# Optimization experiments

Hardware: AMD Instinct MI355X
Metric: run time of the kernel (lower is better)

Reference implementation:

```python
import jax, jax.numpy as jnp
import numpy as np

B, D, H, W, C = 2, 8, 64, 64, 128
NH = 8
WS = (2, 8, 8)
SS = (1, 4, 4)
HEAD_DIM = C // NH
SCALE = HEAD_DIM ** -0.5
MLP_HIDDEN = 4 * C


def _window_partition(x, ws):
    # x: (B, D, H, W, C) -> (B*nW, ws0*ws1*ws2, C)
    b, d, h, w, c = x.shape
    x = x.reshape(b, d // ws[0], ws[0], h // ws[1], ws[1], w // ws[2], ws[2], c)
    return x.transpose(0, 1, 3, 5, 2, 4, 6, 7).reshape(-1, ws[0] * ws[1] * ws[2], c)


def _window_reverse(win, ws, b, d, h, w):
    x = win.reshape(b, d // ws[0], h // ws[1], w // ws[2], ws[0], ws[1], ws[2], -1)
    return x.transpose(0, 1, 4, 2, 5, 3, 6, 7).reshape(b, d, h, w, -1)


def _rel_pos_index(ws):
    coords = np.stack(np.meshgrid(np.arange(ws[0]), np.arange(ws[1]), np.arange(ws[2]), indexing='ij'))
    cf = coords.reshape(3, -1)                       # (3, N)
    rel = (cf[:, :, None] - cf[:, None, :]).transpose(1, 2, 0)  # (N, N, 3)
    rel[:, :, 0] += ws[0] - 1
    rel[:, :, 1] += ws[1] - 1
    rel[:, :, 2] += ws[2] - 1
    rel[:, :, 0] *= (2 * ws[1] - 1) * (2 * ws[2] - 1)
    rel[:, :, 1] *= 2 * ws[2] - 1
    return rel.sum(-1)                               # (N, N)


def _attn_mask(d, h, w, ws, ss):
    img = np.zeros((1, d, h, w, 1), np.float32)
    cnt = 0
    for sd in (slice(-ws[0]), slice(-ws[0], -ss[0]), slice(-ss[0], None)):
        for sh in (slice(-ws[1]), slice(-ws[1], -ss[1]), slice(-ss[1], None)):
            for sw in (slice(-ws[2]), slice(-ws[2], -ss[2]), slice(-ss[2], None)):
                img[:, sd, sh, sw, :] = cnt
                cnt += 1
    mw = _window_partition(img, ws)[..., 0]          # (nW, N)
    am = mw[:, None, :] - mw[:, :, None]             # (nW, N, N)
    return np.where(am != 0, -100.0, 0.0).astype(np.float32)


def _ln(x, g, b):
    m = x.mean(-1, keepdims=True)
    v = ((x - m) ** 2).mean(-1, keepdims=True)
    return (x - m) / jnp.sqrt(v + 1e-5) * g + b


def setup_inputs() -> dict:
    key = jax.random.key(0)
    ks = jax.random.split(key, 8)
    n_bias = (2 * WS[0] - 1) * (2 * WS[1] - 1) * (2 * WS[2] - 1)
    return {
        'x': jax.random.normal(ks[0], (B, D, H, W, C), jnp.float32),
        'qkv_w': jax.random.normal(ks[1], (3 * C, C), jnp.float32) * 0.02,
        'qkv_b': jnp.zeros((3 * C,), jnp.float32),
        'proj_w': jax.random.normal(ks[2], (C, C), jnp.float32) * 0.02,
        'proj_b': jnp.zeros((C,), jnp.float32),
        'rpb': jax.random.normal(ks[3], (n_bias, NH), jnp.float32) * 0.02,
        'ln1_g': jnp.ones((C,), jnp.float32),
        'ln1_b': jnp.zeros((C,), jnp.float32),
        'ln2_g': jnp.ones((C,), jnp.float32),
        'ln2_b': jnp.zeros((C,), jnp.float32),
        'fc1_w': jax.random.normal(ks[4], (MLP_HIDDEN, C), jnp.float32) * 0.02,
        'fc1_b': jnp.zeros((MLP_HIDDEN,), jnp.float32),
        'fc2_w': jax.random.normal(ks[5], (C, MLP_HIDDEN), jnp.float32) * 0.02,
        'fc2_b': jnp.zeros((C,), jnp.float32),
    }


def reference(x, qkv_w, qkv_b, proj_w, proj_b, rpb, ln1_g, ln1_b, ln2_g, ln2_b, fc1_w, fc1_b, fc2_w, fc2_b):
    shortcut = x
    xn = _ln(x, ln1_g, ln1_b)
    # cyclic shift (SW-MSA)
    xs = jnp.roll(xn, (-SS[0], -SS[1], -SS[2]), axis=(1, 2, 3))
    win = _window_partition(xs, WS)                  # (Bw, N, C)
    Bw, N, _ = win.shape
    qkv = (win @ qkv_w.T + qkv_b).reshape(Bw, N, 3, NH, HEAD_DIM).transpose(2, 0, 3, 1, 4)
    q, k, v = qkv[0] * SCALE, qkv[1], qkv[2]         # (Bw, NH, N, d)
    attn = jnp.einsum('bhnd,bhmd->bhnm', q, k)       # (Bw, NH, N, N)
    rpi = _rel_pos_index(WS)
    bias = rpb[rpi.reshape(-1)].reshape(N, N, NH).transpose(2, 0, 1)  # (NH, N, N)
    attn = attn + bias[None]
    mask = jnp.asarray(_attn_mask(D, H, W, WS, SS))  # (nW, N, N)
    nW = mask.shape[0]
    attn = attn.reshape(B, nW, NH, N, N) + mask[None, :, None]
    attn = jax.nn.softmax(attn, axis=-1).reshape(Bw, NH, N, N)
    out = jnp.einsum('bhnm,bhmd->bhnd', attn, v).transpose(0, 2, 1, 3).reshape(Bw, N, C)
    out = out @ proj_w.T + proj_b
    xr = _window_reverse(out, WS, B, D, H, W)
    xr = jnp.roll(xr, SS, axis=(1, 2, 3))
    x1 = shortcut + xr
    # MLP block
    y = _ln(x1, ln2_g, ln2_b)
    y = jax.nn.gelu(y @ fc1_w.T + fc1_b, approximate=False)
    y = y @ fc2_w.T + fc2_b
    return x1 + y
```

## Files before the change

### kernel.cpp

```cpp
#include <hip/hip_runtime.h>
#include <math.h>

typedef short s16x8 __attribute__((ext_vector_type(8)));
typedef float f32x4 __attribute__((ext_vector_type(4)));

#define MFMA(a, b, c)   __builtin_amdgcn_mfma_f32_16x16x32_bf16(a, b, c, 0, 0, 0)

__device__ __forceinline__ float b2f(ushort u) {
    union { unsigned int i; float f; } v; v.i = ((unsigned int)u) << 16; return v.f;
}
__device__ __forceinline__ ushort f2b(float f) {
    union { float f; unsigned int i; } v; v.f = f;
    unsigned int r = v.i + 0x7fffu + ((v.i >> 16) & 1u);
    return (ushort)(r >> 16);
}
__device__ __forceinline__ float gelu_tanh(float v) {
    float u = 0.7978845608f * (v + 0.044715f * v * v * v);
    float e = __expf(-2.f * fabsf(u));
    float t = (1.f - e) / (1.f + e);
    t = (u < 0.f) ? -t : t;
    return 0.5f * v * (1.f + t);
}

__global__ __launch_bounds__(256) void k0_prep(
    const float* __restrict__ qkv_w, const float* __restrict__ proj_w,
    const float* __restrict__ fc1_w, const float* __restrict__ fc2_w,
    const float* __restrict__ rpb, ushort* __restrict__ wq,
    ushort* __restrict__ wp, ushort* __restrict__ wf, ushort* __restrict__ bm)
{
    int bid = blockIdx.x, tid = threadIdx.x;
    if (bid < 192) { int idx = bid * 256 + tid; wq[idx] = f2b(qkv_w[idx]); return; }
    if (bid < 256) { int idx = (bid - 192) * 256 + tid; wp[idx] = f2b(proj_w[idx]); return; }
    if (bid < 768) {
        int idx = (bid - 256) * 256 + tid;
        wf[idx] = f2b(idx < 65536 ? fc1_w[idx] : fc2_w[idx - 65536]);
        return;
    }
    int bi = bid - 768;
    int cls = bi >> 3, head = bi & 7;
    int ed = (cls >> 2) & 1, eh = (cls >> 1) & 1, ew = cls & 1;
    int j = tid & 127;
    int tdj = j >> 6, thj = (j >> 3) & 7, twj = j & 7;
    int regj = (ed ? (tdj + 1) : 0) * 9
             + (eh ? ((thj < 4) ? 1 : 2) : 0) * 3
             + (ew ? ((twj < 4) ? 1 : 2) : 0);
    ushort* bmp = bm + (long)bi * 16384;
    for (int ii = 0; ii < 64; ++ii) {
        int i = (tid >> 7) * 64 + ii;
        int tdi = i >> 6, thi = (i >> 3) & 7, twi = i & 7;
        int regi = (ed ? (tdi + 1) : 0) * 9
                 + (eh ? ((thi < 4) ? 1 : 2) : 0) * 3
                 + (ew ? ((twi < 4) ? 1 : 2) : 0);
        int rpi = (tdi - tdj + 1) * 225 + (thi - thj + 7) * 15 + (twi - twj + 7);
        float v = rpb[rpi * 8 + head] + ((regi != regj) ? -100.f : 0.f);
        bmp[i * 128 + j] = f2b(v);
    }
}

__global__ __launch_bounds__(256) void k2_qkv(
    const float* __restrict__ x, const float* __restrict__ g,
    const float* __restrict__ be, const ushort* __restrict__ wq,
    const float* __restrict__ qkv_b, ushort* __restrict__ qkv)
{
    __shared__ __align__(16) ushort As[128][136];
    int tid = threadIdx.x;
    int m0 = blockIdx.x * 128;
    {
        int row = tid >> 1, half = tid & 1;
        int tk = m0 + row;
        int wi = tk >> 7, t = tk & 127;
        int b = wi >> 8, wd = (wi >> 6) & 3, wh = (wi >> 3) & 7, ww = wi & 7;
        int td = t >> 6, th = (t >> 3) & 7, tw = t & 7;
        int d = (wd * 2 + td + 1) & 7;
        int h = (wh * 8 + th + 4) & 63;
        int w = (ww * 8 + tw + 4) & 63;
        long src = (((long)((b * 8 + d) * 64 + h)) * 64 + w) * 128 + half * 64;
        float vals[64];
        float s = 0.f, q = 0.f;
        #pragma unroll
        for (int i = 0; i < 16; ++i) {
            float4 u = *(const float4*)&x[src + i * 4];
            vals[i * 4 + 0] = u.x; vals[i * 4 + 1] = u.y;
            vals[i * 4 + 2] = u.z; vals[i * 4 + 3] = u.w;
            s += u.x + u.y + u.z + u.w;
            q += u.x * u.x + u.y * u.y + u.z * u.z + u.w * u.w;
        }
        s += __shfl_xor(s, 1);
        q += __shfl_xor(q, 1);
        float mean = s * (1.f / 128.f);
        float rstd = rsqrtf(q * (1.f / 128.f) - mean * mean + 1e-5f);
        #pragma unroll
        for (int i = 0; i < 8; ++i) {
            ushort pk[8];
            #pragma unroll
            for (int jj = 0; jj < 8; ++jj) {
                int c = half * 64 + i * 8 + jj;
                pk[jj] = f2b((vals[i * 8 + jj] - mean) * rstd * g[c] + be[c]);
            }
            *(uint4*)&As[row][half * 64 + i * 8] = *(uint4*)pk;
        }
    }
    __syncthreads();
    int wv = tid >> 6, lane = tid & 63, li = lane & 15, quad = lane >> 4;
    int wm = wv >> 1, wn = wv & 1;
    long wibase = (long)(m0 >> 7) * 49152;
    for (int nb = 0; nb < 3; ++nb) {
        f32x4 acc[4][4] = {};
        for (int s = 0; s < 4; ++s) {
            s16x8 a[4], bw[4];
            #pragma unroll
            for (int mi = 0; mi < 4; ++mi)
                a[mi] = *(const s16x8*)&As[wm * 64 + mi * 16 + li][s * 32 + quad * 8];
            #pragma unroll
            for (int ni = 0; ni < 4; ++ni)
                bw[ni] = *(const s16x8*)&wq[(long)(nb * 128 + wn * 64 + ni * 16 + li) * 128
                                            + s * 32 + quad * 8];
            #pragma unroll
            for (int mi = 0; mi < 4; ++mi)
                #pragma unroll
                for (int ni = 0; ni < 4; ++ni)
                    acc[mi][ni] = MFMA(a[mi], bw[ni], acc[mi][ni]);
        }
        #pragma unroll
        for (int mi = 0; mi < 4; ++mi)
            #pragma unroll
            for (int ni = 0; ni < 4; ++ni) {
                int gcol = nb * 128 + wn * 64 + ni * 16 + li;
                int mat = gcol >> 7, hd = (gcol >> 4) & 7;
                float bias = qkv_b[gcol];
                float scale = (mat == 0) ? 0.25f : 1.f;
                long base2 = wibase + mat * 16384 + hd * 2048 + li;
                #pragma unroll
                for (int r = 0; r < 4; ++r) {
                    int trow = wm * 64 + mi * 16 + quad * 4 + r;
                    qkv[base2 + trow * 16] = f2b((acc[mi][ni][r] + bias) * scale);
                }
            }
    }
}

__global__ __launch_bounds__(256) void k3_attn(
    ushort* __restrict__ qkv, const ushort* __restrict__ bm)
{
    __shared__ __align__(16) ushort qs[128][40];
    __shared__ __align__(16) ushort ks[128][40];
    __shared__ __align__(16) ushort vt[16][136];
    __shared__ __align__(16) ushort ps[128][136];
    int wi = blockIdx.x;
    int wd = (wi >> 6) & 3, wh = (wi >> 3) & 7, ww = wi & 7;
    int cls = ((wd == 3) << 2) | ((wh == 7) << 1) | (ww == 7);
    int tid = threadIdx.x;
    int wv = tid >> 6, lane = tid & 63, li = lane & 15, quad = lane >> 4;
    long wbase = (long)wi * 49152;
    uint2 opk[8][2];
    for (int h = 0; h < 8; ++h) {
        __syncthreads();
        {   int token = tid >> 1, dd0 = (tid & 1) * 8;
            long tb = wbase + h * 2048 + token * 16 + dd0;
            uint4 qv = *(const uint4*)&qkv[tb];
            uint4 kv = *(const uint4*)&qkv[tb + 16384];
            uint4 vv = *(const uint4*)&qkv[tb + 32768];
            uint4 z = {0, 0, 0, 0};
            *(uint4*)&qs[token][dd0] = qv;
            *(uint4*)&ks[token][dd0] = kv;
            *(uint4*)&qs[token][16 + dd0] = z;
            *(uint4*)&ks[token][16 + dd0] = z;
            const ushort* pv = (const ushort*)&vv;
            #pragma unroll
            for (int j = 0; j < 8; ++j) vt[dd0 + j][token] = pv[j];
        }
        __syncthreads();
        f32x4 sacc[2][8] = {};
        s16x8 a[2];
        #pragma unroll
        for (int mi = 0; mi < 2; ++mi)
            a[mi] = *(const s16x8*)&qs[wv * 32 + mi * 16 + li][quad * 8];
        #pragma unroll
        for (int ni = 0; ni < 8; ++ni) {
            s16x8 bf = *(const s16x8*)&ks[ni * 16 + li][quad * 8];
            #pragma unroll
            for (int mi = 0; mi < 2; ++mi) sacc[mi][ni] = MFMA(a[mi], bf, sacc[mi][ni]);
        }
        long bmbase = (long)(cls * 8 + h) * 16384;
        #pragma unroll
        for (int mi = 0; mi < 2; ++mi) {
            #pragma unroll
            for (int r = 0; r < 4; ++r) {
                int i = wv * 32 + mi * 16 + quad * 4 + r;
                float sv[8];
                float rowmax = -1e30f;
                #pragma unroll
                for (int ni = 0; ni < 8; ++ni) {
                    float v = sacc[mi][ni][r] + b2f(bm[bmbase + i * 128 + ni * 16 + li]);
                    sv[ni] = v;
                    rowmax = fmaxf(rowmax, v);
                }
                #pragma unroll
                for (int m = 1; m < 16; m <<= 1) rowmax = fmaxf(rowmax, __shfl_xor(rowmax, m));
                float sum = 0.f;
                #pragma unroll
                for (int ni = 0; ni < 8; ++ni) { sv[ni] = __expf(sv[ni] - rowmax); sum += sv[ni]; }
                #pragma unroll
                for (int m = 1; m < 16; m <<= 1) sum += __shfl_xor(sum, m);
                float inv = 1.f / sum;
                #pragma unroll
                for (int ni = 0; ni < 8; ++ni) ps[i][ni * 16 + li] = f2b(sv[ni] * inv);
            }
        }
        __syncthreads();
        f32x4 pacc[2] = {};
        #pragma unroll
        for (int kk = 0; kk < 4; ++kk) {
            s16x8 bv = *(const s16x8*)&vt[li][kk * 32 + quad * 8];
            #pragma unroll
            for (int mi = 0; mi < 2; ++mi) {
                s16x8 ap = *(const s16x8*)&ps[wv * 32 + mi * 16 + li][kk * 32 + quad * 8];
                pacc[mi] = MFMA(ap, bv, pacc[mi]);
            }
        }
        #pragma unroll
        for (int mi = 0; mi < 2; ++mi) {
            opk[h][mi].x = (unsigned int)f2b(pacc[mi][0]) | ((unsigned int)f2b(pacc[mi][1]) << 16);
            opk[h][mi].y = (unsigned int)f2b(pacc[mi][2]) | ((unsigned int)f2b(pacc[mi][3]) << 16);
        }
    }
    #pragma unroll
    for (int h = 0; h < 8; ++h)
        #pragma unroll
        for (int mi = 0; mi < 2; ++mi) {
            unsigned int w0 = opk[h][mi].x, w1 = opk[h][mi].y;
            #pragma unroll
            for (int r = 0; r < 4; ++r) {
                unsigned int word = (r < 2) ? w0 : w1;
                ushort v = (ushort)((word >> ((r & 1) * 16)) & 0xffff);
                int i = wv * 32 + mi * 16 + quad * 4 + r;
                qkv[wbase + (long)i * 128 + h * 16 + li] = v;
            }
        }
}

__global__ __launch_bounds__(256) void k45(
    const ushort* __restrict__ ao, const ushort* __restrict__ wp,
    const float* __restrict__ proj_b, const float* __restrict__ x,
    const float* __restrict__ g2, const float* __restrict__ be2,
    const ushort* __restrict__ wf1, const float* __restrict__ fc1_b,
    const ushort* __restrict__ wf2, const float* __restrict__ fc2_b,
    float* __restrict__ out)
{
    __shared__ __align__(16) ushort As[64][132];
    __shared__ __align__(16) ushort x1t[64][132];
    __shared__ __align__(16) ushort hs[64][132];
    __shared__ float redS[4][64];
    __shared__ float redQ[4][64];
    int tid = threadIdx.x;
    int b = blockIdx.x;
    int wi = b >> 1, half64 = b & 1;
    int wd = (wi >> 6) & 3, wh = (wi >> 3) & 7, ww = wi & 7;
    int bb = wi >> 8;
    long aobase = (long)wi * 49152 + half64 * 8192;
    #pragma unroll
    for (int i = 0; i < 4; ++i) {
        int slot = tid + i * 256;
        int row = slot >> 4, c8 = (slot & 15) * 8;
        *(uint4*)&As[row][c8] = *(const uint4*)&ao[aobase + row * 128 + c8];
    }
    __syncthreads();
    int wv = tid >> 6, lane = tid & 63, li = lane & 15, quad = lane >> 4;
    int wm = wv >> 1, wn = wv & 1;
    f32x4 acc[2][4] = {};
    for (int s = 0; s < 4; ++s) {
        s16x8 a[2], bw[4];
        #pragma unroll
        for (int mi = 0; mi < 2; ++mi)
            a[mi] = *(const s16x8*)&As[wm * 32 + mi * 16 + li][s * 32 + quad * 8];
        #pragma unroll
        for (int ni = 0; ni < 4; ++ni)
            bw[ni] = *(const s16x8*)&wp[(long)(wn * 64 + ni * 16 + li) * 128 + s * 32 + quad * 8];
        #pragma unroll
        for (int mi = 0; mi < 2; ++mi)
            #pragma unroll
            for (int ni = 0; ni < 4; ++ni)
                acc[mi][ni] = MFMA(a[mi], bw[ni], acc[mi][ni]);
    }
    #pragma unroll
    for (int mi = 0; mi < 2; ++mi) {
        #pragma unroll
        for (int r = 0; r < 4; ++r) {
            int lrow = wm * 32 + mi * 16 + quad * 4 + r;
            int t = half64 * 64 + lrow;
            int td = t >> 6, th = (t >> 3) & 7, tw = t & 7;
            int d = (wd * 2 + td + 1) & 7, h = (wh * 8 + th + 4) & 63, w = (ww * 8 + tw + 4) & 63;
            long di = (((long)((bb * 8 + d) * 64 + h)) * 64 + w) * 128;
            #pragma unroll
            for (int ni = 0; ni < 4; ++ni) {
                int col = wn * 64 + ni * 16 + li;
                x1t[lrow][col] = f2b(acc[mi][ni][r] + proj_b[col] + x[di + col]);
            }
        }
    }
    __syncthreads();
    {
        int token = tid & 63, part = tid >> 6;
        float vals[32];
        float s = 0.f, q = 0.f;
        #pragma unroll
        for (int i = 0; i < 4; ++i) {
            uint4 u = *(const uint4*)&x1t[token][part * 32 + i * 8];
            const ushort* p = (const ushort*)&u;
            #pragma unroll
            for (int j = 0; j < 8; ++j) { float f = b2f(p[j]); vals[i * 8 + j] = f; s += f; q += f * f; }
        }
        redS[part][token] = s; redQ[part][token] = q;
        __syncthreads();
        float st = 0.f, qt = 0.f;
        #pragma unroll
        for (int p2 = 0; p2 < 4; ++p2) { st += redS[p2][token]; qt += redQ[p2][token]; }
        float mean = st * (1.f / 128.f);
        float rstd = rsqrtf(qt * (1.f / 128.f) - mean * mean + 1e-5f);
        #pragma unroll
        for (int i = 0; i < 4; ++i) {
            ushort packed[8];
            #pragma unroll
            for (int j = 0; j < 8; ++j) {
                int c = part * 32 + i * 8 + j;
                packed[j] = f2b((vals[i * 8 + j] - mean) * rstd * g2[c] + be2[c]);
            }
            *(uint4*)&As[token][part * 32 + i * 8] = *(uint4*)packed;
        }
    }
    __syncthreads();
    f32x4 yacc[2][4] = {};
    for (int hc = 0; hc < 4; ++hc) {
        f32x4 hacc[2][4] = {};
        #pragma unroll
        for (int kk = 0; kk < 4; ++kk) {
            s16x8 a[2], bw[4];
            #pragma unroll
            for (int mi = 0; mi < 2; ++mi)
                a[mi] = *(const s16x8*)&As[wm * 32 + mi * 16 + li][kk * 32 + quad * 8];
            #pragma unroll
            for (int ni = 0; ni < 4; ++ni)
                bw[ni] = *(const s16x8*)&wf1[(long)(hc * 128 + wn * 64 + ni * 16 + li) * 128
                                             + kk * 32 + quad * 8];
            #pragma unroll
            for (int mi = 0; mi < 2; ++mi)
                #pragma unroll
                for (int ni = 0; ni < 4; ++ni)
                    hacc[mi][ni] = MFMA(a[mi], bw[ni], hacc[mi][ni]);
        }
        #pragma unroll
        for (int mi = 0; mi < 2; ++mi)
            #pragma unroll
            for (int ni = 0; ni < 4; ++ni) {
                int col = wn * 64 + ni * 16 + li;
                float bbv = fc1_b[hc * 128 + col];
                #pragma unroll
                for (int r = 0; r < 4; ++r) {
                    int row = wm * 32 + mi * 16 + quad * 4 + r;
                    hs[row][col] = f2b(gelu_tanh(hacc[mi][ni][r] + bbv));
                }
            }
        __syncthreads();
        #pragma unroll
        for (int kk = 0; kk < 4; ++kk) {
            s16x8 a[2], bw[4];
            #pragma unroll
            for (int mi = 0; mi < 2; ++mi)
                a[mi] = *(const s16x8*)&hs[wm * 32 + mi * 16 + li][kk * 32 + quad * 8];
            #pragma unroll
            for (int ni = 0; ni < 4; ++ni)
                bw[ni] = *(const s16x8*)&wf2[(long)(wn * 64 + ni * 16 + li) * 512
                                             + hc * 128 + kk * 32 + quad * 8];
            #pragma unroll
            for (int mi = 0; mi < 2; ++mi)
                #pragma unroll
                for (int ni = 0; ni < 4; ++ni)
                    yacc[mi][ni] = MFMA(a[mi], bw[ni], yacc[mi][ni]);
        }
        __syncthreads();
    }
    #pragma unroll
    for (int mi = 0; mi < 2; ++mi) {
        #pragma unroll
        for (int r = 0; r < 4; ++r) {
            int lrow = wm * 32 + mi * 16 + quad * 4 + r;
            int t = half64 * 64 + lrow;
            int td = t >> 6, th = (t >> 3) & 7, tw = t & 7;
            int d = (wd * 2 + td + 1) & 7, h = (wh * 8 + th + 4) & 63, w = (ww * 8 + tw + 4) & 63;
            long di = (((long)((bb * 8 + d) * 64 + h)) * 64 + w) * 128;
            #pragma unroll
            for (int ni = 0; ni < 4; ++ni) {
                int col = wn * 64 + ni * 16 + li;
                out[di + col] = b2f(x1t[lrow][col]) + yacc[mi][ni][r] + fc2_b[col];
            }
        }
    }
}

extern "C" void kernel_launch(void* const* d_in, const int* in_sizes, int n_in,
                              void* d_out, int out_size, void* d_ws, size_t ws_size,
                              hipStream_t stream)
{
    (void)in_sizes; (void)n_in; (void)out_size; (void)ws_size;
    const float* x      = (const float*)d_in[0];
    const float* qkv_w  = (const float*)d_in[1];
    const float* qkv_b  = (const float*)d_in[2];
    const float* proj_w = (const float*)d_in[3];
    const float* proj_b = (const float*)d_in[4];
    const float* rpb    = (const float*)d_in[5];
    const float* ln1_g  = (const float*)d_in[6];
    const float* ln1_b  = (const float*)d_in[7];
    const float* ln2_g  = (const float*)d_in[8];
    const float* ln2_b  = (const float*)d_in[9];
    const float* fc1_w  = (const float*)d_in[10];
    const float* fc1_b  = (const float*)d_in[11];
    const float* fc2_w  = (const float*)d_in[12];
    const float* fc2_b  = (const float*)d_in[13];
    float* out = (float*)d_out;

    ushort* qkvb = (ushort*)d_ws;
    ushort* wq   = (ushort*)((char*)d_ws + 50331648);
    ushort* wp   = wq + 49152;
    ushort* wf   = wp + 16384;
    ushort* bm   = wf + 131072;

    hipLaunchKernelGGL(k0_prep, dim3(832), dim3(256), 0, stream,
                       qkv_w, proj_w, fc1_w, fc2_w, rpb, wq, wp, wf, bm);
    hipLaunchKernelGGL(k2_qkv, dim3(512), dim3(256), 0, stream,
                       x, ln1_g, ln1_b, wq, qkv_b, qkvb);
    hipLaunchKernelGGL(k3_attn, dim3(512), dim3(256), 0, stream, qkvb, bm);
    hipLaunchKernelGGL(k45, dim3(1024), dim3(256), 0, stream,
                       qkvb, wp, proj_b, x, ln2_g, ln2_b,
                       wf, fc1_b, wf + 65536, fc2_b, out);
}
```

Baseline: 286.5 us.

## Compute LN2 stats from MFMA registers and keep x1 in registers

The proj+MLP kernel now computes the residual x1 in MFMA accumulator registers and reduces LayerNorm sums with wavefront shuffles plus a small shared buffer, instead of staging x1 through a shared tile and re-reading it. x1 is kept packed as bf16 in registers for the final residual add. The x1t shared array is removed and launch bounds request 4 blocks per CU. This cuts shared memory use and one sync, aiming at higher occupancy, but register pressure rises and spills become possible under the 4-block bound.

```diff
diff --git a/kernel.cpp b/kernel.cpp
--- a/kernel.cpp
+++ b/kernel.cpp
@@ -239,7 +239,7 @@
         }
 }
 
-__global__ __launch_bounds__(256) void k45(
+__global__ __launch_bounds__(256, 4) void k45(
     const ushort* __restrict__ ao, const ushort* __restrict__ wp,
     const float* __restrict__ proj_b, const float* __restrict__ x,
     const float* __restrict__ g2, const float* __restrict__ be2,
@@ -248,10 +248,9 @@
     float* __restrict__ out)
 {
     __shared__ __align__(16) ushort As[64][132];
-    __shared__ __align__(16) ushort x1t[64][132];
     __shared__ __align__(16) ushort hs[64][132];
-    __shared__ float redS[4][64];
-    __shared__ float redQ[4][64];
+    __shared__ float redS[2][64];
+    __shared__ float redQ[2][64];
     int tid = threadIdx.x;
     int b = blockIdx.x;
     int wi = b >> 1, half64 = b & 1;
@@ -282,52 +281,67 @@
             for (int ni = 0; ni < 4; ++ni)
                 acc[mi][ni] = MFMA(a[mi], bw[ni], acc[mi][ni]);
     }
+    int cols[4];
     #pragma unroll
-    for (int mi = 0; mi < 2; ++mi) {
-        #pragma unroll
-        for (int r = 0; r < 4; ++r) {
-            int lrow = wm * 32 + mi * 16 + quad * 4 + r;
-            int t = half64 * 64 + lrow;
-            int td = t >> 6, th = (t >> 3) & 7, tw = t & 7;
-            int d = (wd * 2 + td + 1) & 7, h = (wh * 8 + th + 4) & 63, w = (ww * 8 + tw + 4) & 63;
-            long di = (((long)((bb * 8 + d) * 64 + h)) * 64 + w) * 128;
-            #pragma unroll
-            for (int ni = 0; ni < 4; ++ni) {
-                int col = wn * 64 + ni * 16 + li;
-                x1t[lrow][col] = f2b(acc[mi][ni][r] + proj_b[col] + x[di + col]);
+    for (int ni = 0; ni < 4; ++ni) cols[ni] = wn * 64 + ni * 16 + li;
+    {
+        float pbv[4];
+        #pragma unroll
+        for (int ni = 0; ni < 4; ++ni) pbv[ni] = proj_b[cols[ni]];
+        #pragma unroll
+        for (int mi = 0; mi < 2; ++mi) {
+            #pragma unroll
+            for (int r = 0; r < 4; ++r) {
+                int lrow = wm * 32 + mi * 16 + quad * 4 + r;
+                int t = half64 * 64 + lrow;
+                int td = t >> 6, th = (t >> 3) & 7, tw = t & 7;
+                int d = (wd * 2 + td + 1) & 7, h = (wh * 8 + th + 4) & 63, w = (ww * 8 + tw + 4) & 63;
+                long di = (((long)((bb * 8 + d) * 64 + h)) * 64 + w) * 128;
+                float s_ = 0.f, q_ = 0.f;
+                #pragma unroll
+                for (int ni = 0; ni < 4; ++ni) {
+                    float v = acc[mi][ni][r] + pbv[ni] + x[di + cols[ni]];
+                    acc[mi][ni][r] = v;
+                    s_ += v; q_ += v * v;
+                }
+                #pragma unroll
+                for (int m = 1; m < 16; m <<= 1) {
+                    s_ += __shfl_xor(s_, m);
+                    q_ += __shfl_xor(q_, m);
+                }
+                if (li == 0) { redS[wn][lrow] = s_; redQ[wn][lrow] = q_; }
             }
         }
     }
     __syncthreads();
     {
-        int token = tid & 63, part = tid >> 6;
-        float vals[32];
-        float s = 0.f, q = 0.f;
-        #pragma unroll
-        for (int i = 0; i < 4; ++i) {
-            uint4 u = *(const uint4*)&x1t[token][part * 32 + i * 8];
-            const ushort* p = (const ushort*)&u;
-            #pragma unroll
-            for (int j = 0; j < 8; ++j) { float f = b2f(p[j]); vals[i * 8 + j] = f; s += f; q += f * f; }
-        }
-        redS[part][token] = s; redQ[part][token] = q;
-        __syncthreads();
-        float st = 0.f, qt = 0.f;
-        #pragma unroll
-        for (int p2 = 0; p2 < 4; ++p2) { st += redS[p2][token]; qt += redQ[p2][token]; }
-        float mean = st * (1.f / 128.f);
-        float rstd = rsqrtf(qt * (1.f / 128.f) - mean * mean + 1e-5f);
-        #pragma unroll
-        for (int i = 0; i < 4; ++i) {
-            ushort packed[8];
-            #pragma unroll
-            for (int j = 0; j < 8; ++j) {
-                int c = part * 32 + i * 8 + j;
-                packed[j] = f2b((vals[i * 8 + j] - mean) * rstd * g2[c] + be2[c]);
-            }
-            *(uint4*)&As[token][part * 32 + i * 8] = *(uint4*)packed;
-        }
-    }
+        float g2v[4], be2v[4];
+        #pragma unroll
+        for (int ni = 0; ni < 4; ++ni) { g2v[ni] = g2[cols[ni]]; be2v[ni] = be2[cols[ni]]; }
+        #pragma unroll
+        for (int mi = 0; mi < 2; ++mi) {
+            #pragma unroll
+            for (int r = 0; r < 4; ++r) {
+                int lrow = wm * 32 + mi * 16 + quad * 4 + r;
+                float tS = redS[0][lrow] + redS[1][lrow];
+                float tQ = redQ[0][lrow] + redQ[1][lrow];
+                float mean = tS * (1.f / 128.f);
+                float rstd = rsqrtf(tQ * (1.f / 128.f) - mean * mean + 1e-5f);
+                #pragma unroll
+                for (int ni = 0; ni < 4; ++ni)
+                    As[lrow][cols[ni]] = f2b((acc[mi][ni][r] - mean) * rstd * g2v[ni] + be2v[ni]);
+            }
+        }
+    }
+    uint x1p[2][4][2];
+    #pragma unroll
+    for (int mi = 0; mi < 2; ++mi)
+        #pragma unroll
+        for (int ni = 0; ni < 4; ++ni)
+            #pragma unroll
+            for (int rr = 0; rr < 2; ++rr)
+                x1p[mi][ni][rr] = (unsigned int)f2b(acc[mi][ni][2 * rr])
+                                | ((unsigned int)f2b(acc[mi][ni][2 * rr + 1]) << 16);
     __syncthreads();
     f32x4 yacc[2][4] = {};
     for (int hc = 0; hc < 4; ++hc) {
@@ -379,19 +393,25 @@
         }
         __syncthreads();
     }
-    #pragma unroll
-    for (int mi = 0; mi < 2; ++mi) {
-        #pragma unroll
-        for (int r = 0; r < 4; ++r) {
-            int lrow = wm * 32 + mi * 16 + quad * 4 + r;
-            int t = half64 * 64 + lrow;
-            int td = t >> 6, th = (t >> 3) & 7, tw = t & 7;
-            int d = (wd * 2 + td + 1) & 7, h = (wh * 8 + th + 4) & 63, w = (ww * 8 + tw + 4) & 63;
-            long di = (((long)((bb * 8 + d) * 64 + h)) * 64 + w) * 128;
-            #pragma unroll
-            for (int ni = 0; ni < 4; ++ni) {
-                int col = wn * 64 + ni * 16 + li;
-                out[di + col] = b2f(x1t[lrow][col]) + yacc[mi][ni][r] + fc2_b[col];
+    {
+        float f2v[4];
+        #pragma unroll
+        for (int ni = 0; ni < 4; ++ni) f2v[ni] = fc2_b[cols[ni]];
+        #pragma unroll
+        for (int mi = 0; mi < 2; ++mi) {
+            #pragma unroll
+            for (int r = 0; r < 4; ++r) {
+                int lrow = wm * 32 + mi * 16 + quad * 4 + r;
+                int t = half64 * 64 + lrow;
+                int td = t >> 6, th = (t >> 3) & 7, tw = t & 7;
+                int d = (wd * 2 + td + 1) & 7, h = (wh * 8 + th + 4) & 63, w = (ww * 8 + tw + 4) & 63;
+                long di = (((long)((bb * 8 + d) * 64 + h)) * 64 + w) * 128;
+                #pragma unroll
+                for (int ni = 0; ni < 4; ++ni) {
+                    unsigned int wrd = x1p[mi][ni][r >> 1];
+                    float x1v = b2f((ushort)((wrd >> ((r & 1) * 16)) & 0xffffu));
+                    out[di + cols[ni]] = x1v + yacc[mi][ni][r] + f2v[ni];
+                }
             }
         }
     }
```

After: 304.5 us. 6.3% more time.
